# Optimization experiments

Hardware: AMD Instinct MI355X
Metric: run time of the kernel (lower is better)

Reference implementation:

```python
import jax, jax.numpy as jnp
import numpy as np

B, N, D, PS = 8, 64, 64, 4          # batch, patches, per-patch dim, pooling size (N must equal D)
C_IN, LTF, LTI, LTO = 512, 512, 512, 512
L = D // PS


def setup_inputs() -> dict:
    key = jax.random.key(0)
    ks = jax.random.split(key, 7)
    s = 0.02
    return {
        "x": jax.random.normal(ks[0], (B, N * D, C_IN), dtype=jnp.float32),
        "W_in": jax.random.normal(ks[1], (C_IN, 3 * LTF), dtype=jnp.float32) * s,
        "b_in": jax.random.normal(ks[2], (3 * LTF,), dtype=jnp.float32) * s,
        "W_inter": jax.random.normal(ks[3], (LTF, LTI), dtype=jnp.float32) * s,
        "b_inter": jax.random.normal(ks[4], (LTI,), dtype=jnp.float32) * s,
        "W_last": jax.random.normal(ks[5], (LTI, LTO), dtype=jnp.float32) * s,
        "b_last": jax.random.normal(ks[6], (LTO,), dtype=jnp.float32) * s,
    }


def _lin(t, W, b):
    # channel-wise Linear on [B, C, N, d] maps (permute->Linear->permute fused into one einsum)
    return jnp.einsum('bcnd,ck->bknd', t, W) + b[None, :, None, None]


def reference(x, W_in, b_in, W_inter, b_inter, W_last, b_last):
    # seq2spatial: [B, N*d, C] -> [B, C, N, d]
    xs = jnp.transpose(x.reshape(B, N, D, C_IN), (0, 3, 1, 2))

    qkv = _lin(xs, W_in, b_in)                       # [B, 3*ltf, N, d]
    Q, K, V = jnp.split(qkv, 3, axis=1)              # each [B, ltf, N, d]

    def pool(t):  # avg_pool1d over N with kernel=stride=PS
        return t.reshape(B, t.shape[1], N // PS, PS, D).mean(axis=3)

    q = pool(Q)                                      # [B, ltf, L, d]
    k = pool(K)                                      # [B, ltf, L, d]

    def inter_last(t):
        # latent_inter_: Linear + softmax over channel dim; latent_last_: Linear (identity act)
        t = jax.nn.softmax(_lin(t, W_inter, b_inter), axis=1)
        return _lin(t, W_last, b_last)

    Qk = inter_last(jnp.einsum('bcnd,bcld->bcnl', Q, k))   # [B, lto, N, L]
    qK = inter_last(jnp.einsum('bcld,bcnd->bcln', q, K))   # [B, lto, L, N]
    Vp = inter_last(V)                                     # [B, lto, N, d]

    qKV = jnp.einsum('bcln,bcnd->bcld', qK, Vp)            # [B, lto, L, d]
    return jnp.einsum('bcnl,bcld->bcnd', Qk, qKV)          # [B, lto, N, d]
```

## Files before the change

kernel.cpp:

```cpp
#include <hip/hip_runtime.h>

typedef unsigned short u16;
typedef __attribute__((ext_vector_type(8))) short s16x8;
typedef __attribute__((ext_vector_type(4))) short s16x4;
typedef __attribute__((ext_vector_type(4))) float f32x4;

__device__ __forceinline__ u16 f2bf(float f){
  union { float f; unsigned u; } v; v.f = f;
  unsigned r = v.u + 0x7FFFu + ((v.u >> 16) & 1u);
  return (u16)(r >> 16);
}
__device__ __forceinline__ float bf2f(u16 h){
  union { unsigned u; float f; } v; v.u = ((unsigned)h) << 16;
  return v.f;
}
__device__ __forceinline__ f32x4 mfma16(s16x8 a, s16x8 b, f32x4 c){
  return __builtin_amdgcn_mfma_f32_16x16x32_bf16(a, b, c, 0, 0, 0);
}
__device__ __forceinline__ void gload16(const void* g, void* l){
  __builtin_amdgcn_global_load_lds((const __attribute__((address_space(1))) void*)g,
                                   (__attribute__((address_space(3))) void*)l, 16, 0, 0);
}
__device__ __forceinline__ int flidx(int k, int c){
  return ((k >> 4) * 16 + (c >> 5)) * 512 + ((c >> 3) & 3) * 128 + (k & 15) * 8 + (c & 7);
}

__global__ __launch_bounds__(256) void k0w(
    const float* __restrict__ W_in, const float* __restrict__ W_inter, const float* __restrict__ W_last,
    u16* __restrict__ WT_in, u16* __restrict__ WTi_rm, u16* __restrict__ WiFL, u16* __restrict__ WlFL)
{
  const int t = blockIdx.x * 256 + threadIdx.x;
  if (t < 1024 * 512){ const int k = t >> 9, c = t & 511; WT_in[t] = f2bf(W_in[c * 1536 + k]); }
  if (t < 512 * 512){
    const int k = t >> 9, c = t & 511;
    const int fl = flidx(k, c);
    const u16 wi = f2bf(W_inter[c * 512 + k]);
    WTi_rm[t] = wi;
    WiFL[fl]  = wi;
    WlFL[fl]  = f2bf(W_last[c * 512 + k]);
  }
}

__global__ __launch_bounds__(256) void k0x(const float* __restrict__ x, u16* __restrict__ xb)
{
  const int t = blockIdx.x * 256 + threadIdx.x;
  const f32x4* src = (const f32x4*)x + (size_t)t * 2;
  f32x4 a = src[0], b = src[1];
  alignas(16) u16 h[8];
  #pragma unroll
  for (int i = 0; i < 4; ++i){ h[i] = f2bf(a[i]); h[4 + i] = f2bf(b[i]); }
  *(s16x8*)&xb[(size_t)t * 8] = *(const s16x8*)h;
}

__global__ __launch_bounds__(256) void k0b_wvi(
    const float* __restrict__ W_in, const float* __restrict__ W_inter,
    const u16* __restrict__ WTi_rm, const float* __restrict__ b_in, const float* __restrict__ b_inter,
    u16* __restrict__ WviFL, float* __restrict__ b_vi)
{
  __shared__ u16 A_lds[64][72];
  if (blockIdx.x >= 16){
    float* r = (float*)&A_lds[0][0];
    const int k = (blockIdx.x - 16) * 64 + (threadIdx.x & 63);
    const int pt = threadIdx.x >> 6;
    float s = 0.f;
    #pragma unroll 4
    for (int c = pt * 128; c < pt * 128 + 128; ++c)
      s += b_in[1024 + c] * W_inter[c * 512 + k];
    r[pt * 64 + (threadIdx.x & 63)] = s;
    __syncthreads();
    if (pt == 0){
      const int kk = threadIdx.x;
      b_vi[k] = b_inter[k] + r[kk] + r[64 + kk] + r[128 + kk] + r[192 + kk];
    }
    return;
  }
  const int kt = blockIdx.x & 1;
  const int m0 = (blockIdx.x >> 1) * 64;
  const int tid = threadIdx.x;
  const int w = tid >> 6, l = tid & 63;
  const int l15 = l & 15, lg = l >> 4;
  const int kbase = kt * 256 + w * 64;
  f32x4 acc[4][4] = {};
  const int sr = tid >> 2, sc = (tid & 3) * 16;
  for (int c0 = 0; c0 < 512; c0 += 64){
    __syncthreads();
    {
      const f32x4* src = (const f32x4*)(W_in + (size_t)(m0 + sr) * 1536 + 1024 + c0 + sc);
      f32x4 a0 = src[0], a1 = src[1], a2 = src[2], a3 = src[3];
      alignas(16) u16 h[16];
      #pragma unroll
      for (int i = 0; i < 4; ++i){ h[i] = f2bf(a0[i]); h[4+i] = f2bf(a1[i]); h[8+i] = f2bf(a2[i]); h[12+i] = f2bf(a3[i]); }
      *(s16x8*)&A_lds[sr][sc]     = *(const s16x8*)&h[0];
      *(s16x8*)&A_lds[sr][sc + 8] = *(const s16x8*)&h[8];
    }
    __syncthreads();
    #pragma unroll
    for (int kk = 0; kk < 2; ++kk){
      s16x8 af[4];
      #pragma unroll
      for (int m = 0; m < 4; ++m)
        af[m] = *(const s16x8*)&A_lds[m * 16 + l15][kk * 32 + lg * 8];
      #pragma unroll
      for (int kc = 0; kc < 4; ++kc){
        s16x8 bf = *(const s16x8*)&WTi_rm[(size_t)(kbase + kc * 16 + l15) * 512 + c0 + kk * 32 + lg * 8];
        #pragma unroll
        for (int m = 0; m < 4; ++m) acc[m][kc] = mfma16(af[m], bf, acc[m][kc]);
      }
    }
  }
  #pragma unroll
  for (int kc = 0; kc < 4; ++kc){
    const int k = kbase + kc * 16 + l15;
    #pragma unroll
    for (int m = 0; m < 4; ++m){
      const int cin = m0 + m * 16 + lg * 4;
      uint2 pk;
      pk.x = (unsigned)f2bf(acc[m][kc][0]) | ((unsigned)f2bf(acc[m][kc][1]) << 16);
      pk.y = (unsigned)f2bf(acc[m][kc][2]) | ((unsigned)f2bf(acc[m][kc][3]) << 16);
      *(uint2*)&WviFL[flidx(k, cin)] = pk;
    }
  }
}

__global__ __launch_bounds__(256) void k1_qk(
    const u16* __restrict__ xb, const u16* __restrict__ WT_in, const float* __restrict__ b_in,
    u16* __restrict__ Qp, u16* __restrict__ Kp)
{
  __shared__ __align__(16) u16 As[128 * 64];
  __shared__ __align__(16) u16 Bs[128 * 64];
  const int t = threadIdx.x;
  const int w = t >> 6, l = t & 63;
  const int l15 = l & 15, lg = l >> 4;
  const int wr = w >> 1, wc = w & 1;
  const size_t Mbase = (size_t)blockIdx.y * 128;
  const int Nbase = blockIdx.x * 128;

  f32x4 acc[4][4] = {};
  for (int c0 = 0; c0 < 512; c0 += 64){
    __syncthreads();
    #pragma unroll
    for (int it = 0; it < 4; ++it){
      const int g = it * 256 + t;
      const int row = g >> 3, cc = g & 7;
      const int sc = (cc ^ (row & 7)) * 8;
      gload16(&xb[(Mbase + row) * 512 + c0 + sc], &As[g * 8]);
    }
    #pragma unroll
    for (int it = 0; it < 4; ++it){
      const int g = it * 256 + t;
      const int row = g >> 3, cc = g & 7;
      const int sc = (cc ^ (row & 7)) * 8;
      gload16(&WT_in[(size_t)(Nbase + row) * 512 + c0 + sc], &Bs[g * 8]);
    }
    __syncthreads();
    #pragma unroll
    for (int kk = 0; kk < 2; ++kk){
      s16x8 af[4], bf[4];
      #pragma unroll
      for (int m = 0; m < 4; ++m){
        const int row = wr * 64 + m * 16 + l15;
        af[m] = *(const s16x8*)&As[row * 64 + ((kk * 4 + lg) ^ (row & 7)) * 8];
      }
      #pragma unroll
      for (int n = 0; n < 4; ++n){
        const int row = wc * 64 + n * 16 + l15;
        bf[n] = *(const s16x8*)&Bs[row * 64 + ((kk * 4 + lg) ^ (row & 7)) * 8];
      }
      #pragma unroll
      for (int n = 0; n < 4; ++n)
        #pragma unroll
        for (int m = 0; m < 4; ++m) acc[m][n] = mfma16(af[m], bf[n], acc[m][n]);
    }
  }
  const int b = (int)(Mbase >> 12);
  const int ploc = ((int)Mbase & 4095) + wr * 64;
  #pragma unroll
  for (int n = 0; n < 4; ++n){
    const int kglob = Nbase + wc * 64 + n * 16 + l15;
    const float bias = b_in[kglob];
    u16* dst = (kglob < 512) ? Qp : Kp;
    const int kq = kglob & 511;
    #pragma unroll
    for (int m = 0; m < 4; ++m){
      const int p = ploc + m * 16 + lg * 4;
      uint2 pk;
      pk.x = (unsigned)f2bf(acc[m][n][0] + bias) | ((unsigned)f2bf(acc[m][n][1] + bias) << 16);
      pk.y = (unsigned)f2bf(acc[m][n][2] + bias) | ((unsigned)f2bf(acc[m][n][3] + bias) << 16);
      *(uint2*)&dst[((size_t)b * 512 + kq) * 4096 + p] = pk;
    }
  }
}

__global__ __launch_bounds__(256) void k2_pool(
    const u16* __restrict__ Qp, const u16* __restrict__ Kp,
    u16* __restrict__ qp, u16* __restrict__ kp)
{
  const int t = blockIdx.x * 256 + threadIdx.x;
  const int i = t & 0x7FFFF;
  const u16* src = (t >> 19) ? Kp : Qp;
  u16* dst = (t >> 19) ? kp : qp;
  const int d8 = i & 7, lp = (i >> 3) & 15, c = (i >> 7) & 511, b = (i >> 16) & 7;
  const size_t base = ((size_t)b * 512 + c) * 4096 + lp * 256 + d8 * 8;
  float s[8] = {};
  #pragma unroll
  for (int r = 0; r < 4; ++r){
    s16x8 v = *(const s16x8*)&src[base + r * 64];
    #pragma unroll
    for (int e = 0; e < 8; ++e) s[e] += bf2f((u16)v[e]);
  }
  alignas(16) u16 h[8];
  #pragma unroll
  for (int e = 0; e < 8; ++e) h[e] = f2bf(s[e] * 0.25f);
  *(s16x8*)&dst[((size_t)b * 512 + c) * 1024 + lp * 64 + d8 * 8] = *(const s16x8*)h;
}

__global__ __launch_bounds__(512) void k3_scores(
    const u16* __restrict__ Qp, const u16* __restrict__ kp,
    const u16* __restrict__ qp, const u16* __restrict__ Kp,
    u16* __restrict__ T12)
{
  __shared__ __align__(16) u16 buf[1024 * 20];
  const bool s2 = blockIdx.x >= 256;
  const int blk = blockIdx.x & 255;
  const int b = blk >> 5, c0 = (blk & 31) * 16;
  const int w = threadIdx.x >> 6;
  const int l = threadIdx.x & 63, l15 = l & 15, lg = l >> 4;
  #pragma unroll
  for (int half = 0; half < 2; ++half){
    const int c = c0 + half * 8 + w;
    const int cc = half * 8 + w;
    if (!s2){
      const u16* Qr = Qp + ((size_t)b * 512 + c) * 4096;
      const u16* kr = kp + ((size_t)b * 512 + c) * 1024;
      f32x4 acc[4] = {};
      #pragma unroll
      for (int kk = 0; kk < 2; ++kk){
        s16x8 bf = *(const s16x8*)&kr[l15 * 64 + kk * 32 + lg * 8];
        #pragma unroll
        for (int m = 0; m < 4; ++m){
          s16x8 af = *(const s16x8*)&Qr[(m * 16 + l15) * 64 + kk * 32 + lg * 8];
          acc[m] = mfma16(af, bf, acc[m]);
        }
      }
      #pragma unroll
      for (int m = 0; m < 4; ++m)
        #pragma unroll
        for (int j = 0; j < 4; ++j)
          buf[((m * 16 + lg * 4 + j) * 16 + l15) * 20 + cc] = f2bf(acc[m][j]);
    } else {
      const u16* qr = qp + ((size_t)b * 512 + c) * 1024;
      const u16* Kr = Kp + ((size_t)b * 512 + c) * 4096;
      f32x4 acc[4] = {};
      #pragma unroll
      for (int kk = 0; kk < 2; ++kk){
        s16x8 af = *(const s16x8*)&qr[l15 * 64 + kk * 32 + lg * 8];
        #pragma unroll
        for (int nt = 0; nt < 4; ++nt){
          s16x8 bf = *(const s16x8*)&Kr[(nt * 16 + l15) * 64 + kk * 32 + lg * 8];
          acc[nt] = mfma16(af, bf, acc[nt]);
        }
      }
      #pragma unroll
      for (int nt = 0; nt < 4; ++nt)
        #pragma unroll
        for (int j = 0; j < 4; ++j)
          buf[((lg * 4 + j) * 64 + nt * 16 + l15) * 20 + cc] = f2bf(acc[nt][j]);
    }
  }
  __syncthreads();
  const int off = s2 ? 1024 : 0;
  for (int rr = (int)threadIdx.x; rr < 1024; rr += 512){
    uint2 a  = *(const uint2*)&buf[rr * 20 + 0];
    uint2 bq = *(const uint2*)&buf[rr * 20 + 4];
    uint2 cq = *(const uint2*)&buf[rr * 20 + 8];
    uint2 dq = *(const uint2*)&buf[rr * 20 + 12];
    u16* dst = &T12[((size_t)b * 2048 + off + rr) * 512 + c0];
    *(uint4*)&dst[0] = make_uint4(a.x, a.y, bq.x, bq.y);
    *(uint4*)&dst[8] = make_uint4(cq.x, cq.y, dq.x, dq.y);
  }
}

__global__ __launch_bounds__(512) void k4_interlast(
    const u16* __restrict__ T, u16* __restrict__ O,
    const u16* __restrict__ WiFL, const float* __restrict__ bi,
    const u16* __restrict__ WlFL, const float* __restrict__ bl, const int Pn)
{
  __shared__ __align__(16) u16 smem[64 * 512];
  float* red = (float*)smem;
  const int b = blockIdx.y;
  const int p0 = blockIdx.x * 64;
  const int w = threadIdx.x >> 6, l = threadIdx.x & 63;
  const int l15 = l & 15, lg = l >> 4;
  const u16* Tb = T + (size_t)b * Pn * 512;

  #pragma unroll
  for (int it = 0; it < 8; ++it){
    const int g = it * 512 + threadIdx.x;
    const int row = g >> 6, cc = g & 63;
    const int sc = ((cc & 7) ^ (row & 7)) | (cc & 56);
    gload16(&Tb[(size_t)(p0 + row) * 512 + sc * 8], &smem[g * 8]);
  }
  __syncthreads();

  f32x4 acc[4][4] = {};
  for (int cs = 0; cs < 16; ++cs){
    s16x8 af[4];
    #pragma unroll
    for (int pr = 0; pr < 4; ++pr){
      const int row = pr * 16 + l15;
      const int gi = cs * 4 + lg;
      const int gs = ((gi & 7) ^ (row & 7)) | (gi & 56);
      af[pr] = *(const s16x8*)&smem[row * 512 + gs * 8];
    }
    #pragma unroll
    for (int kc = 0; kc < 4; ++kc){
      s16x8 bf = *(const s16x8*)&WiFL[(size_t)(((w * 4 + kc) * 16 + cs) * 64 + l) * 8];
      #pragma unroll
      for (int pr = 0; pr < 4; ++pr) acc[pr][kc] = mfma16(af[pr], bf, acc[pr][kc]);
    }
  }
  __syncthreads();

  #pragma unroll
  for (int kc = 0; kc < 4; ++kc){
    const float bias = bi[w * 64 + kc * 16 + l15];
    #pragma unroll
    for (int pr = 0; pr < 4; ++pr)
      #pragma unroll
      for (int j = 0; j < 4; ++j)
        acc[pr][kc][j] = __expf(acc[pr][kc][j] + bias);
  }
  #pragma unroll
  for (int pr = 0; pr < 4; ++pr)
    #pragma unroll
    for (int j = 0; j < 4; ++j){
      float s = (acc[pr][0][j] + acc[pr][1][j]) + (acc[pr][2][j] + acc[pr][3][j]);
      s += __shfl_xor(s, 1); s += __shfl_xor(s, 2);
      s += __shfl_xor(s, 4); s += __shfl_xor(s, 8);
      if (l15 == 0) red[(pr * 16 + lg * 4 + j) * 8 + w] = s;
    }
  __syncthreads();
  float inv[4][4];
  {
    const f32x4* r = (const f32x4*)&red[l * 8];
    f32x4 r0 = r[0], r1 = r[1];
    float S = ((r0[0] + r0[1]) + (r0[2] + r0[3])) + ((r1[0] + r1[1]) + (r1[2] + r1[3]));
    #pragma unroll
    for (int pr = 0; pr < 4; ++pr)
      #pragma unroll
      for (int j = 0; j < 4; ++j)
        inv[pr][j] = 1.f / __shfl(S, pr * 16 + lg * 4 + j);
  }
  __syncthreads();
  #pragma unroll
  for (int pr = 0; pr < 4; ++pr)
    #pragma unroll
    for (int j = 0; j < 4; ++j){
      const int row = pr * 16 + lg * 4 + j;
      const int sw = (row & 7) << 3;
      #pragma unroll
      for (int kc = 0; kc < 4; ++kc)
        smem[row * 512 + ((w * 64 + kc * 16 + l15) ^ sw)] = f2bf(acc[pr][kc][j]);
    }
  __syncthreads();
  f32x4 z[4][4] = {};
  const int swr = (l15 & 7) << 3;
  for (int ks = 0; ks < 16; ++ks){
    const int k0 = ks * 32 + lg * 8;
    s16x8 af[4];
    #pragma unroll
    for (int pr = 0; pr < 4; ++pr)
      af[pr] = *(const s16x8*)&smem[(pr * 16 + l15) * 512 + (k0 ^ swr)];
    #pragma unroll
    for (int kc = 0; kc < 4; ++kc){
      s16x8 bf = *(const s16x8*)&WlFL[(size_t)(((w * 4 + kc) * 16 + ks) * 64 + l) * 8];
      #pragma unroll
      for (int pr = 0; pr < 4; ++pr) z[pr][kc] = mfma16(af[pr], bf, z[pr][kc]);
    }
  }
  u16* Ob = O + (size_t)b * 512 * Pn;
  #pragma unroll
  for (int kc = 0; kc < 4; ++kc){
    const int k2 = w * 64 + kc * 16 + l15;
    const float bias = bl[k2];
    #pragma unroll
    for (int pr = 0; pr < 4; ++pr){
      uint2 pk;
      pk.x = (unsigned)f2bf(z[pr][kc][0] * inv[pr][0] + bias) | ((unsigned)f2bf(z[pr][kc][1] * inv[pr][1] + bias) << 16);
      pk.y = (unsigned)f2bf(z[pr][kc][2] * inv[pr][2] + bias) | ((unsigned)f2bf(z[pr][kc][3] * inv[pr][3] + bias) << 16);
      *(uint2*)&Ob[(size_t)k2 * Pn + p0 + pr * 16 + lg * 4] = pk;
    }
  }
}

__global__ __launch_bounds__(256) void k56(
    const u16* __restrict__ O12, const u16* __restrict__ Vp, float* __restrict__ out)
{
  __shared__ __align__(16) u16 Vt[4][64 * 68];
  __shared__ __align__(16) u16 Tt[4][16 * 64];
  const int w = threadIdx.x >> 6;
  const int W = blockIdx.x * 4 + w;
  const int b = W >> 9, c = W & 511;
  const int l = threadIdx.x & 63, l15 = l & 15, lg = l >> 4;
  const u16* base = O12 + ((size_t)b * 512 + c) * 2048;
  const u16* Qr = base;
  const u16* qr = base + 1024;
  const u16* vr = Vp + ((size_t)b * 512 + c) * 4096;
  u16* vt = &Vt[w][0];
  u16* tt = &Tt[w][0];
  {
    const s16x8* src = (const s16x8*)&vr[l * 64];
    #pragma unroll
    for (int i = 0; i < 8; ++i){
      s16x8 v = src[i];
      *(s16x4*)&vt[l * 68 + i * 8]     = __builtin_shufflevector(v, v, 0, 1, 2, 3);
      *(s16x4*)&vt[l * 68 + i * 8 + 4] = __builtin_shufflevector(v, v, 4, 5, 6, 7);
    }
  }
  f32x4 acc1[4] = {};
  #pragma unroll
  for (int kk = 0; kk < 2; ++kk){
    s16x8 af = *(const s16x8*)&qr[l15 * 64 + kk * 32 + lg * 8];
    #pragma unroll
    for (int dt = 0; dt < 4; ++dt){
      alignas(16) u16 bh[8];
      #pragma unroll
      for (int j = 0; j < 8; ++j)
        bh[j] = vt[(kk * 32 + lg * 8 + j) * 68 + dt * 16 + l15];
      acc1[dt] = mfma16(af, *(const s16x8*)bh, acc1[dt]);
    }
  }
  #pragma unroll
  for (int dt = 0; dt < 4; ++dt)
    #pragma unroll
    for (int j = 0; j < 4; ++j)
      tt[(lg * 4 + j) * 64 + dt * 16 + l15] = f2bf(acc1[dt][j]);
  s16x8 af2[4] = {};
  if (lg < 2){
    #pragma unroll
    for (int m = 0; m < 4; ++m)
      af2[m] = *(const s16x8*)&Qr[(m * 16 + l15) * 16 + lg * 8];
  }
  f32x4 acc2[4][4] = {};
  #pragma unroll
  for (int dt = 0; dt < 4; ++dt){
    alignas(16) u16 bh[8] = {};
    if (lg < 2){
      #pragma unroll
      for (int j = 0; j < 8; ++j)
        bh[j] = tt[(lg * 8 + j) * 64 + dt * 16 + l15];
    }
    s16x8 bf = *(const s16x8*)bh;
    #pragma unroll
    for (int m = 0; m < 4; ++m) acc2[m][dt] = mfma16(af2[m], bf, acc2[m][dt]);
  }
  float* ob = out + ((size_t)b * 512 + c) * 4096;
  #pragma unroll
  for (int m = 0; m < 4; ++m)
    #pragma unroll
    for (int dt = 0; dt < 4; ++dt)
      #pragma unroll
      for (int j = 0; j < 4; ++j)
        ob[(m * 16 + lg * 4 + j) * 64 + dt * 16 + l15] = acc2[m][dt][j];
}

extern "C" void kernel_launch(void* const* d_in, const int* in_sizes, int n_in,
                              void* d_out, int out_size, void* d_ws, size_t ws_size,
                              hipStream_t stream)
{
  (void)in_sizes; (void)n_in; (void)out_size; (void)ws_size;
  const float* x       = (const float*)d_in[0];
  const float* W_in    = (const float*)d_in[1];
  const float* b_in    = (const float*)d_in[2];
  const float* W_inter = (const float*)d_in[3];
  const float* b_inter = (const float*)d_in[4];
  const float* W_last  = (const float*)d_in[5];
  const float* b_last  = (const float*)d_in[6];
  float* out = (float*)d_out;

  char* ws = (char*)d_ws;
  size_t off = 0;
  auto alloc = [&](size_t bytes) -> u16* {
    u16* p = (u16*)(ws + off);
    off += (bytes + 255) & ~(size_t)255;
    return p;
  };
  u16*  WT_in  = alloc((size_t)1024 * 512 * 2);
  u16*  WTi_rm = alloc((size_t)512 * 512 * 2);
  u16*  WiFL   = alloc((size_t)512 * 512 * 2);
  u16*  WlFL   = alloc((size_t)512 * 512 * 2);
  u16*  WviFL  = alloc((size_t)512 * 512 * 2);
  float* b_vi  = (float*)alloc((size_t)512 * 4);
  u16*  xb     = alloc((size_t)8 * 4096 * 512 * 2);
  u16*  Qp     = alloc((size_t)8 * 512 * 4096 * 2);
  u16*  Kp     = alloc((size_t)8 * 512 * 4096 * 2);
  u16*  qp     = alloc((size_t)8 * 512 * 1024 * 2);
  u16*  kp     = alloc((size_t)8 * 512 * 1024 * 2);
  u16*  T12    = alloc((size_t)8 * 2048 * 512 * 2);
  u16*  Vpp    = Qp;
  u16*  O12    = xb;

  k0w<<<2048, 256, 0, stream>>>(W_in, W_inter, W_last, WT_in, WTi_rm, WiFL, WlFL);
  k0x<<<8192, 256, 0, stream>>>(x, xb);
  k0b_wvi<<<24, 256, 0, stream>>>(W_in, W_inter, WTi_rm, b_in, b_inter, WviFL, b_vi);
  k1_qk<<<dim3(8, 256), 256, 0, stream>>>(xb, WT_in, b_in, Qp, Kp);
  k2_pool<<<4096, 256, 0, stream>>>(Qp, Kp, qp, kp);
  k3_scores<<<512, 512, 0, stream>>>(Qp, kp, qp, Kp, T12);
  k4_interlast<<<dim3(64, 8), 512, 0, stream>>>(xb, Vpp, WviFL, b_vi, WlFL, b_last, 4096);
  k4_interlast<<<dim3(32, 8), 512, 0, stream>>>(T12, O12, WiFL, b_inter, WlFL, b_last, 2048);
  k56<<<1024, 256, 0, stream>>>(O12, Vpp, out);
}
```

Baseline: 387.4 us.

## Fuse pooling into score kernel, merge prep and interlast launches, prefetch weights

Removes the separate pooling kernel by averaging the four K or Q rows on the fly inside the score kernel, which drops the qp/kp intermediate buffers. Merges the weight and x conversion kernels into one launch and the two inter/last launches into one grid. The V and score blocks share that grid, with O12 now aliased to Kp. Inside the inter/last kernel, weight fragments are software-prefetched one step ahead, and one barrier is removed by giving the softmax reduction its own shared buffer. The cost is redundant pooling loads in the score kernel, more registers, and a larger shared-memory footprint.

```diff
diff --git a/kernel.cpp b/kernel.cpp
--- a/kernel.cpp
+++ b/kernel.cpp
@@ -25,31 +25,31 @@
   return ((k >> 4) * 16 + (c >> 5)) * 512 + ((c >> 3) & 3) * 128 + (k & 15) * 8 + (c & 7);
 }
 
-__global__ __launch_bounds__(256) void k0w(
+__global__ __launch_bounds__(256) void k0prep(
     const float* __restrict__ W_in, const float* __restrict__ W_inter, const float* __restrict__ W_last,
-    u16* __restrict__ WT_in, u16* __restrict__ WTi_rm, u16* __restrict__ WiFL, u16* __restrict__ WlFL)
-{
-  const int t = blockIdx.x * 256 + threadIdx.x;
-  if (t < 1024 * 512){ const int k = t >> 9, c = t & 511; WT_in[t] = f2bf(W_in[c * 1536 + k]); }
-  if (t < 512 * 512){
-    const int k = t >> 9, c = t & 511;
-    const int fl = flidx(k, c);
-    const u16 wi = f2bf(W_inter[c * 512 + k]);
-    WTi_rm[t] = wi;
-    WiFL[fl]  = wi;
-    WlFL[fl]  = f2bf(W_last[c * 512 + k]);
-  }
-}
-
-__global__ __launch_bounds__(256) void k0x(const float* __restrict__ x, u16* __restrict__ xb)
-{
-  const int t = blockIdx.x * 256 + threadIdx.x;
-  const f32x4* src = (const f32x4*)x + (size_t)t * 2;
-  f32x4 a = src[0], b = src[1];
-  alignas(16) u16 h[8];
-  #pragma unroll
-  for (int i = 0; i < 4; ++i){ h[i] = f2bf(a[i]); h[4 + i] = f2bf(b[i]); }
-  *(s16x8*)&xb[(size_t)t * 8] = *(const s16x8*)h;
+    u16* __restrict__ WT_in, u16* __restrict__ WTi_rm, u16* __restrict__ WiFL, u16* __restrict__ WlFL,
+    const float* __restrict__ x, u16* __restrict__ xb)
+{
+  if (blockIdx.x < 2048){
+    const int t = blockIdx.x * 256 + threadIdx.x;
+    if (t < 1024 * 512){ const int k = t >> 9, c = t & 511; WT_in[t] = f2bf(W_in[c * 1536 + k]); }
+    if (t < 512 * 512){
+      const int k = t >> 9, c = t & 511;
+      const int fl = flidx(k, c);
+      const u16 wi = f2bf(W_inter[c * 512 + k]);
+      WTi_rm[t] = wi;
+      WiFL[fl]  = wi;
+      WlFL[fl]  = f2bf(W_last[c * 512 + k]);
+    }
+  } else {
+    const int t = (blockIdx.x - 2048) * 256 + threadIdx.x;
+    const f32x4* src = (const f32x4*)x + (size_t)t * 2;
+    f32x4 a = src[0], b = src[1];
+    alignas(16) u16 h[8];
+    #pragma unroll
+    for (int i = 0; i < 4; ++i){ h[i] = f2bf(a[i]); h[4 + i] = f2bf(b[i]); }
+    *(s16x8*)&xb[(size_t)t * 8] = *(const s16x8*)h;
+  }
 }
 
 __global__ __launch_bounds__(256) void k0b_wvi(
@@ -191,33 +191,8 @@
   }
 }
 
-__global__ __launch_bounds__(256) void k2_pool(
-    const u16* __restrict__ Qp, const u16* __restrict__ Kp,
-    u16* __restrict__ qp, u16* __restrict__ kp)
-{
-  const int t = blockIdx.x * 256 + threadIdx.x;
-  const int i = t & 0x7FFFF;
-  const u16* src = (t >> 19) ? Kp : Qp;
-  u16* dst = (t >> 19) ? kp : qp;
-  const int d8 = i & 7, lp = (i >> 3) & 15, c = (i >> 7) & 511, b = (i >> 16) & 7;
-  const size_t base = ((size_t)b * 512 + c) * 4096 + lp * 256 + d8 * 8;
-  float s[8] = {};
-  #pragma unroll
-  for (int r = 0; r < 4; ++r){
-    s16x8 v = *(const s16x8*)&src[base + r * 64];
-    #pragma unroll
-    for (int e = 0; e < 8; ++e) s[e] += bf2f((u16)v[e]);
-  }
-  alignas(16) u16 h[8];
-  #pragma unroll
-  for (int e = 0; e < 8; ++e) h[e] = f2bf(s[e] * 0.25f);
-  *(s16x8*)&dst[((size_t)b * 512 + c) * 1024 + lp * 64 + d8 * 8] = *(const s16x8*)h;
-}
-
 __global__ __launch_bounds__(512) void k3_scores(
-    const u16* __restrict__ Qp, const u16* __restrict__ kp,
-    const u16* __restrict__ qp, const u16* __restrict__ Kp,
-    u16* __restrict__ T12)
+    const u16* __restrict__ Qp, const u16* __restrict__ Kp, u16* __restrict__ T12)
 {
   __shared__ __align__(16) u16 buf[1024 * 20];
   const bool s2 = blockIdx.x >= 256;
@@ -228,14 +203,24 @@
   #pragma unroll
   for (int half = 0; half < 2; ++half){
     const int c = c0 + half * 8 + w;
-    const int cc = half * 8 + w;
+    const int ci = half * 8 + w;
+    const u16* Qr = Qp + ((size_t)b * 512 + c) * 4096;
+    const u16* Kr = Kp + ((size_t)b * 512 + c) * 4096;
     if (!s2){
-      const u16* Qr = Qp + ((size_t)b * 512 + c) * 4096;
-      const u16* kr = kp + ((size_t)b * 512 + c) * 1024;
       f32x4 acc[4] = {};
       #pragma unroll
       for (int kk = 0; kk < 2; ++kk){
-        s16x8 bf = *(const s16x8*)&kr[l15 * 64 + kk * 32 + lg * 8];
+        float pv[8] = {};
+        #pragma unroll
+        for (int r = 0; r < 4; ++r){
+          s16x8 v = *(const s16x8*)&Kr[(4 * l15 + r) * 64 + kk * 32 + lg * 8];
+          #pragma unroll
+          for (int j = 0; j < 8; ++j) pv[j] += bf2f((u16)v[j]);
+        }
+        alignas(16) u16 bh[8];
+        #pragma unroll
+        for (int j = 0; j < 8; ++j) bh[j] = f2bf(pv[j] * 0.25f);
+        s16x8 bf = *(const s16x8*)bh;
         #pragma unroll
         for (int m = 0; m < 4; ++m){
           s16x8 af = *(const s16x8*)&Qr[(m * 16 + l15) * 64 + kk * 32 + lg * 8];
@@ -246,14 +231,22 @@
       for (int m = 0; m < 4; ++m)
         #pragma unroll
         for (int j = 0; j < 4; ++j)
-          buf[((m * 16 + lg * 4 + j) * 16 + l15) * 20 + cc] = f2bf(acc[m][j]);
+          buf[((m * 16 + lg * 4 + j) * 16 + l15) * 20 + ci] = f2bf(acc[m][j]);
     } else {
-      const u16* qr = qp + ((size_t)b * 512 + c) * 1024;
-      const u16* Kr = Kp + ((size_t)b * 512 + c) * 4096;
       f32x4 acc[4] = {};
       #pragma unroll
       for (int kk = 0; kk < 2; ++kk){
-        s16x8 af = *(const s16x8*)&qr[l15 * 64 + kk * 32 + lg * 8];
+        float pv[8] = {};
+        #pragma unroll
+        for (int r = 0; r < 4; ++r){
+          s16x8 v = *(const s16x8*)&Qr[(4 * l15 + r) * 64 + kk * 32 + lg * 8];
+          #pragma unroll
+          for (int j = 0; j < 8; ++j) pv[j] += bf2f((u16)v[j]);
+        }
+        alignas(16) u16 ah[8];
+        #pragma unroll
+        for (int j = 0; j < 8; ++j) ah[j] = f2bf(pv[j] * 0.25f);
+        s16x8 af = *(const s16x8*)ah;
         #pragma unroll
         for (int nt = 0; nt < 4; ++nt){
           s16x8 bf = *(const s16x8*)&Kr[(nt * 16 + l15) * 64 + kk * 32 + lg * 8];
@@ -264,7 +257,7 @@
       for (int nt = 0; nt < 4; ++nt)
         #pragma unroll
         for (int j = 0; j < 4; ++j)
-          buf[((lg * 4 + j) * 64 + nt * 16 + l15) * 20 + cc] = f2bf(acc[nt][j]);
+          buf[((lg * 4 + j) * 64 + nt * 16 + l15) * 20 + ci] = f2bf(acc[nt][j]);
     }
   }
   __syncthreads();
@@ -281,14 +274,23 @@
 }
 
 __global__ __launch_bounds__(512) void k4_interlast(
-    const u16* __restrict__ T, u16* __restrict__ O,
-    const u16* __restrict__ WiFL, const float* __restrict__ bi,
-    const u16* __restrict__ WlFL, const float* __restrict__ bl, const int Pn)
+    const u16* __restrict__ TV, const u16* __restrict__ Tab,
+    u16* __restrict__ OV, u16* __restrict__ Oab,
+    const u16* __restrict__ WviFL, const float* __restrict__ b_vi,
+    const u16* __restrict__ WiFL, const float* __restrict__ b_ab,
+    const u16* __restrict__ WlFL, const float* __restrict__ bl)
 {
   __shared__ __align__(16) u16 smem[64 * 512];
-  float* red = (float*)smem;
+  __shared__ __align__(16) float red2[64 * 8];
+  const bool isV = blockIdx.x < 64;
+  const int bx = isV ? (int)blockIdx.x : (int)blockIdx.x - 64;
+  const int Pn = isV ? 4096 : 2048;
+  const u16* T = isV ? TV : Tab;
+  u16* O = isV ? OV : Oab;
+  const u16* W1 = isV ? WviFL : WiFL;
+  const float* bi = isV ? b_vi : b_ab;
   const int b = blockIdx.y;
-  const int p0 = blockIdx.x * 64;
+  const int p0 = bx * 64;
   const int w = threadIdx.x >> 6, l = threadIdx.x & 63;
   const int l15 = l & 15, lg = l >> 4;
   const u16* Tb = T + (size_t)b * Pn * 512;
@@ -303,20 +305,32 @@
   __syncthreads();
 
   f32x4 acc[4][4] = {};
-  for (int cs = 0; cs < 16; ++cs){
-    s16x8 af[4];
-    #pragma unroll
-    for (int pr = 0; pr < 4; ++pr){
-      const int row = pr * 16 + l15;
-      const int gi = cs * 4 + lg;
-      const int gs = ((gi & 7) ^ (row & 7)) | (gi & 56);
-      af[pr] = *(const s16x8*)&smem[row * 512 + gs * 8];
-    }
-    #pragma unroll
-    for (int kc = 0; kc < 4; ++kc){
-      s16x8 bf = *(const s16x8*)&WiFL[(size_t)(((w * 4 + kc) * 16 + cs) * 64 + l) * 8];
-      #pragma unroll
-      for (int pr = 0; pr < 4; ++pr) acc[pr][kc] = mfma16(af[pr], bf, acc[pr][kc]);
+  {
+    s16x8 bfn[4];
+    #pragma unroll
+    for (int kc = 0; kc < 4; ++kc)
+      bfn[kc] = *(const s16x8*)&W1[(size_t)(((w * 4 + kc) * 16) * 64 + l) * 8];
+    for (int cs = 0; cs < 16; ++cs){
+      s16x8 bfc[4];
+      #pragma unroll
+      for (int kc = 0; kc < 4; ++kc) bfc[kc] = bfn[kc];
+      if (cs < 15){
+        #pragma unroll
+        for (int kc = 0; kc < 4; ++kc)
+          bfn[kc] = *(const s16x8*)&W1[(size_t)(((w * 4 + kc) * 16 + cs + 1) * 64 + l) * 8];
+      }
+      s16x8 af[4];
+      #pragma unroll
+      for (int pr = 0; pr < 4; ++pr){
+        const int row = pr * 16 + l15;
+        const int gi = cs * 4 + lg;
+        const int gs = ((gi & 7) ^ (row & 7)) | (gi & 56);
+        af[pr] = *(const s16x8*)&smem[row * 512 + gs * 8];
+      }
+      #pragma unroll
+      for (int kc = 0; kc < 4; ++kc)
+        #pragma unroll
+        for (int pr = 0; pr < 4; ++pr) acc[pr][kc] = mfma16(af[pr], bfc[kc], acc[pr][kc]);
     }
   }
   __syncthreads();
@@ -337,21 +351,8 @@
       float s = (acc[pr][0][j] + acc[pr][1][j]) + (acc[pr][2][j] + acc[pr][3][j]);
       s += __shfl_xor(s, 1); s += __shfl_xor(s, 2);
       s += __shfl_xor(s, 4); s += __shfl_xor(s, 8);
-      if (l15 == 0) red[(pr * 16 + lg * 4 + j) * 8 + w] = s;
-    }
-  __syncthreads();
-  float inv[4][4];
-  {
-    const f32x4* r = (const f32x4*)&red[l * 8];
-    f32x4 r0 = r[0], r1 = r[1];
-    float S = ((r0[0] + r0[1]) + (r0[2] + r0[3])) + ((r1[0] + r1[1]) + (r1[2] + r1[3]));
-    #pragma unroll
-    for (int pr = 0; pr < 4; ++pr)
-      #pragma unroll
-      for (int j = 0; j < 4; ++j)
-        inv[pr][j] = 1.f / __shfl(S, pr * 16 + lg * 4 + j);
-  }
-  __syncthreads();
+      if (l15 == 0) red2[(pr * 16 + lg * 4 + j) * 8 + w] = s;
+    }
   #pragma unroll
   for (int pr = 0; pr < 4; ++pr)
     #pragma unroll
@@ -363,19 +364,43 @@
         smem[row * 512 + ((w * 64 + kc * 16 + l15) ^ sw)] = f2bf(acc[pr][kc][j]);
     }
   __syncthreads();
+
+  float inv[4][4];
+  {
+    const f32x4* r = (const f32x4*)&red2[l * 8];
+    f32x4 r0 = r[0], r1 = r[1];
+    float S = ((r0[0] + r0[1]) + (r0[2] + r0[3])) + ((r1[0] + r1[1]) + (r1[2] + r1[3]));
+    #pragma unroll
+    for (int pr = 0; pr < 4; ++pr)
+      #pragma unroll
+      for (int j = 0; j < 4; ++j)
+        inv[pr][j] = 1.f / __shfl(S, pr * 16 + lg * 4 + j);
+  }
   f32x4 z[4][4] = {};
-  const int swr = (l15 & 7) << 3;
-  for (int ks = 0; ks < 16; ++ks){
-    const int k0 = ks * 32 + lg * 8;
-    s16x8 af[4];
-    #pragma unroll
-    for (int pr = 0; pr < 4; ++pr)
-      af[pr] = *(const s16x8*)&smem[(pr * 16 + l15) * 512 + (k0 ^ swr)];
-    #pragma unroll
-    for (int kc = 0; kc < 4; ++kc){
-      s16x8 bf = *(const s16x8*)&WlFL[(size_t)(((w * 4 + kc) * 16 + ks) * 64 + l) * 8];
-      #pragma unroll
-      for (int pr = 0; pr < 4; ++pr) z[pr][kc] = mfma16(af[pr], bf, z[pr][kc]);
+  {
+    const int swr = (l15 & 7) << 3;
+    s16x8 bfn[4];
+    #pragma unroll
+    for (int kc = 0; kc < 4; ++kc)
+      bfn[kc] = *(const s16x8*)&WlFL[(size_t)(((w * 4 + kc) * 16) * 64 + l) * 8];
+    for (int ks = 0; ks < 16; ++ks){
+      s16x8 bfc[4];
+      #pragma unroll
+      for (int kc = 0; kc < 4; ++kc) bfc[kc] = bfn[kc];
+      if (ks < 15){
+        #pragma unroll
+        for (int kc = 0; kc < 4; ++kc)
+          bfn[kc] = *(const s16x8*)&WlFL[(size_t)(((w * 4 + kc) * 16 + ks + 1) * 64 + l) * 8];
+      }
+      const int k0 = ks * 32 + lg * 8;
+      s16x8 af[4];
+      #pragma unroll
+      for (int pr = 0; pr < 4; ++pr)
+        af[pr] = *(const s16x8*)&smem[(pr * 16 + l15) * 512 + (k0 ^ swr)];
+      #pragma unroll
+      for (int kc = 0; kc < 4; ++kc)
+        #pragma unroll
+        for (int pr = 0; pr < 4; ++pr) z[pr][kc] = mfma16(af[pr], bfc[kc], z[pr][kc]);
     }
   }
   u16* Ob = O + (size_t)b * 512 * Pn;
@@ -494,19 +519,15 @@
   u16*  xb     = alloc((size_t)8 * 4096 * 512 * 2);
   u16*  Qp     = alloc((size_t)8 * 512 * 4096 * 2);
   u16*  Kp     = alloc((size_t)8 * 512 * 4096 * 2);
-  u16*  qp     = alloc((size_t)8 * 512 * 1024 * 2);
-  u16*  kp     = alloc((size_t)8 * 512 * 1024 * 2);
   u16*  T12    = alloc((size_t)8 * 2048 * 512 * 2);
   u16*  Vpp    = Qp;
-  u16*  O12    = xb;
-
-  k0w<<<2048, 256, 0, stream>>>(W_in, W_inter, W_last, WT_in, WTi_rm, WiFL, WlFL);
-  k0x<<<8192, 256, 0, stream>>>(x, xb);
+  u16*  O12    = Kp;
+
+  k0prep<<<10240, 256, 0, stream>>>(W_in, W_inter, W_last, WT_in, WTi_rm, WiFL, WlFL, x, xb);
   k0b_wvi<<<24, 256, 0, stream>>>(W_in, W_inter, WTi_rm, b_in, b_inter, WviFL, b_vi);
   k1_qk<<<dim3(8, 256), 256, 0, stream>>>(xb, WT_in, b_in, Qp, Kp);
-  k2_pool<<<4096, 256, 0, stream>>>(Qp, Kp, qp, kp);
-  k3_scores<<<512, 512, 0, stream>>>(Qp, kp, qp, Kp, T12);
-  k4_interlast<<<dim3(64, 8), 512, 0, stream>>>(xb, Vpp, WviFL, b_vi, WlFL, b_last, 4096);
-  k4_interlast<<<dim3(32, 8), 512, 0, stream>>>(T12, O12, WiFL, b_inter, WlFL, b_last, 2048);
+  k3_scores<<<512, 512, 0, stream>>>(Qp, Kp, T12);
+  k4_interlast<<<dim3(96, 8), 512, 0, stream>>>(xb, T12, Vpp, O12,
+                                                WviFL, b_vi, WiFL, b_inter, WlFL, b_last);
   k56<<<1024, 256, 0, stream>>>(O12, Vpp, out);
 }
```

New measurement: 353.4 us. -8.8%, faster.
